# Performance work log

Measured on AMD Instinct MI355X. Metric: run time of the kernel, lower is better.

Reference implementation:

```python
import jax, jax.numpy as jnp
import numpy as np
from jax import lax


def setup_inputs() -> dict:
    key = jax.random.key(0)
    ks = jax.random.split(key, 9)
    B, Hh, Ww, Cin, Cout, F, E = 8, 64, 64, 256, 256, 128, 256
    s = 0.02  # glorot-ish scale to keep the H->pow(-0.5) chain numerically sane
    return {
        "x": jax.random.normal(ks[0], (B, Hh, Ww, Cin), jnp.float32),
        "w_phi": jax.random.normal(ks[1], (Cin, F), jnp.float32) * s,
        "b_phi": jnp.zeros((F,), jnp.float32),
        "w_a": jax.random.normal(ks[2], (Cin, F), jnp.float32) * s,
        "b_a": jnp.zeros((F,), jnp.float32),
        "w_m": jax.random.normal(ks[3], (7, 7, Cin, E), jnp.float32) * s,
        "b_m": jnp.zeros((E,), jnp.float32),
        "weight_2": jax.random.normal(ks[4], (Cin, Cout), jnp.float32) * s,
        "bias_2": jnp.zeros((Cout,), jnp.float32),
    }


def reference(x, w_phi, b_phi, w_a, b_a, w_m, b_m, weight_2, bias_2):
    B, Hh, Ww, Cin = x.shape
    V = Hh * Ww
    F = w_phi.shape[1]
    E = w_m.shape[-1]

    # phi: 1x1 conv -> [B, V, F]
    phi = (jnp.einsum('bhwc,cf->bhwf', x, w_phi) + b_phi).reshape(B, V, F)

    # A: global average pool + 1x1 conv -> diagonal scale vector [B, F]
    a = jnp.mean(x, axis=(1, 2)) @ w_a + b_a  # (B, F)

    # M: 7x7 SAME conv -> [B, V, E]
    M = lax.conv_general_dilated(
        x, w_m, window_strides=(1, 1), padding='SAME',
        dimension_numbers=('NHWC', 'HWIO', 'NHWC')) + b_m
    M = M.reshape(B, V, E)

    # H = |phi @ diag(a) @ phi^T @ M| without materializing diag(a)
    t = jnp.einsum('bvf,bve->bfe', phi, M)        # phi^T @ M : (B, F, E)
    t = a[:, :, None] * t                          # diag(a) scaling
    Hmat = jnp.abs(jnp.einsum('bvf,bfe->bve', phi, t))  # (B, V, E)

    D = jnp.sum(Hmat, axis=2)                      # vertex degree (B, V)
    D_H = D[:, :, None] ** -0.5 * Hmat             # D^{-1/2} H
    Binv = 1.0 / jnp.sum(Hmat, axis=1)             # edge degree inverse (B, E)

    feats = x.reshape(B, V, Cin)
    tmp = jnp.einsum('bve,bvc->bec', D_H, feats)   # D_H^T @ features
    tmp = Binv[:, :, None] * tmp                   # diag(B^{-1}) scaling
    agg = jnp.einsum('bve,bec->bvc', D_H, tmp)     # D_H @ ...

    out = (feats - agg) @ weight_2 + bias_2        # (B, V, Cout)
    return out.reshape(B, Hh, Ww, -1)
```

## Files before the change

### kernel.cpp

```cpp
#include <hip/hip_runtime.h>
#include <hip/hip_bf16.h>

typedef unsigned short u16;
typedef unsigned int u32;
#define DI __device__ __forceinline__

typedef __attribute__((ext_vector_type(8))) short v8s;
typedef __attribute__((ext_vector_type(4))) float v4f;

constexpr int B_ = 8;
constexpr int V_ = 4096;
constexpr int C_ = 256;
constexpr int F_ = 128;
constexpr int E_ = 256;
constexpr int KK_ = 49;
constexpr int PWS = 80;
constexpr int PS  = 5600;

constexpr size_t OFF_XSUM   = 0;
constexpr size_t OFF_CSUM   = 2048;
constexpr size_t OFF_SPHI   = 4096;
constexpr size_t OFF_A      = 5120;
constexpr size_t OFF_T      = 6144;
constexpr size_t OFF_TMPT   = 268288;
constexpr size_t ZERO_HEAD  = 792576;
constexpr size_t OFF_TT16   = 792576;
constexpr size_t OFF_T2T16  = 923648;
constexpr size_t OFF_W2T16  = 1185792;
constexpr size_t OFF_PHIT   = 1218560;
constexpr size_t OFF_XPT    = 3315712;
constexpr size_t XPT_FLOATS = 5734400;
constexpr size_t OFF_WMT    = 9050112;

DI float bf2f(u16 u) {
    union { u32 i; float f; } v; v.i = ((u32)u) << 16; return v.f;
}
DI u16 f2bf(float f) {
    union { float f; u32 i; } v; v.f = f;
    u32 r = v.i + 0x7fff + ((v.i >> 16) & 1);
    return (u16)(r >> 16);
}

__global__ void k_xsum(const float* __restrict__ x, float* __restrict__ ws) {
    int b = blockIdx.x >> 3;
    int chunk = blockIdx.x & 7;
    int c = threadIdx.x;
    const float* xb = x + ((size_t)b * V_ + chunk * 512) * C_ + c;
    float s = 0.f;
    for (int v = 0; v < 512; ++v) s += xb[(size_t)v * C_];
    atomicAdd(&ws[OFF_XSUM + b * C_ + c], s);
}

__global__ void k_a(const float* __restrict__ w_a, const float* __restrict__ b_a,
                    float* __restrict__ ws) {
    int b = blockIdx.x, f = threadIdx.x;
    float acc = b_a[f];
    const float* xs = &ws[OFF_XSUM + b * C_];
    for (int c = 0; c < C_; ++c)
        acc += (xs[c] * (1.0f / 4096.0f)) * w_a[c * F_ + f];
    ws[OFF_A + b * F_ + f] = acc;
}

__global__ void k_phi(const float* __restrict__ x, const float* __restrict__ w_phi,
                      const float* __restrict__ b_phi, float* __restrict__ ws) {
    __shared__ float xsT[C_][8];
    int r0 = blockIdx.x * 8;
    int b = r0 >> 12;
    int v0 = r0 & 4095;
    int tid = threadIdx.x;
    const float* xb = x + (size_t)r0 * C_;
    for (int i = tid; i < 8 * C_; i += 128) xsT[i & 255][i >> 8] = xb[i];
    __syncthreads();
    int f = tid;
    float bp = b_phi[f];
    float acc[8];
#pragma unroll
    for (int r = 0; r < 8; ++r) acc[r] = bp;
    const float* wp = w_phi + f;
    for (int c = 0; c < C_; ++c) {
        float w = wp[c * F_];
        float4 xa = *(const float4*)&xsT[c][0];
        float4 xb4 = *(const float4*)&xsT[c][4];
        acc[0] += xa.x * w;  acc[1] += xa.y * w;  acc[2] += xa.z * w;  acc[3] += xa.w * w;
        acc[4] += xb4.x * w; acc[5] += xb4.y * w; acc[6] += xb4.z * w; acc[7] += xb4.w * w;
    }
    u16 pb[8];
    float ssum = 0.f;
#pragma unroll
    for (int r = 0; r < 8; ++r) { pb[r] = f2bf(acc[r]); ssum += acc[r]; }
    u16* phiT = (u16*)&ws[OFF_PHIT];
    uint4 q;
    q.x = (u32)pb[0] | ((u32)pb[1] << 16);
    q.y = (u32)pb[2] | ((u32)pb[3] << 16);
    q.z = (u32)pb[4] | ((u32)pb[5] << 16);
    q.w = (u32)pb[6] | ((u32)pb[7] << 16);
    *(uint4*)(phiT + ((size_t)(b * F_ + f)) * V_ + v0) = q;
    atomicAdd(&ws[OFF_SPHI + b * F_ + f], ssum);
}

__global__ void k_padx(const float* __restrict__ x, float* __restrict__ ws) {
    __shared__ float tile[64][68];
    int b = blockIdx.x >> 6;
    int h = blockIdx.x & 63;
    int tid = threadIdx.x;
    u16* xpt = (u16*)&ws[OFF_XPT];
    for (int cc = 0; cc < 4; ++cc) {
        int c0 = cc * 64;
        int w = tid >> 2, q = tid & 3;
        const float* xr = x + ((size_t)(b * V_ + h * 64 + w)) * C_ + c0 + q * 16;
        float4 f0 = *(const float4*)(xr);
        float4 f1 = *(const float4*)(xr + 4);
        float4 f2 = *(const float4*)(xr + 8);
        float4 f3 = *(const float4*)(xr + 12);
        __syncthreads();
        *(float4*)&tile[w][q * 16]      = f0;
        *(float4*)&tile[w][q * 16 + 4]  = f1;
        *(float4*)&tile[w][q * 16 + 8]  = f2;
        *(float4*)&tile[w][q * 16 + 12] = f3;
        __syncthreads();
        int c = tid >> 2, j4 = tid & 3;
        u16* dst = xpt + ((size_t)(b * C_ + c0 + c)) * PS + (h + 3) * PWS + 3 + j4 * 16;
#pragma unroll
        for (int ww = 0; ww < 16; ++ww) dst[ww] = f2bf(tile[j4 * 16 + ww][c]);
    }
}

__global__ void k_wmt(const float* __restrict__ w_m, float* __restrict__ ws) {
    int kk = blockIdx.x;
    int e = threadIdx.x;
    u16* wmt = (u16*)&ws[OFF_WMT];
    for (int c0 = 0; c0 < C_; c0 += 8) {
        u16 pk[8];
#pragma unroll
        for (int i = 0; i < 8; ++i)
            pk[i] = f2bf(w_m[((size_t)kk * C_ + c0 + i) * E_ + e]);
        uint4 q;
        q.x = (u32)pk[0] | ((u32)pk[1] << 16);
        q.y = (u32)pk[2] | ((u32)pk[3] << 16);
        q.z = (u32)pk[4] | ((u32)pk[5] << 16);
        q.w = (u32)pk[6] | ((u32)pk[7] << 16);
        *(uint4*)(wmt + ((size_t)(kk * E_ + e)) * C_ + c0) = q;
    }
}

__global__ void k_w2t(const float* __restrict__ w2, float* __restrict__ ws) {
    int co = blockIdx.x, c = threadIdx.x;
    ((u16*)&ws[OFF_W2T16])[(size_t)co * C_ + c] = f2bf(w2[(size_t)c * C_ + co]);
}

template <int KX>
DI void g1_loop(const u16* __restrict__ phiT_b, const u16* __restrict__ xpt_b,
                int ky, u16* lds_a, u16* lds_b, int tid, v4f acc[4][4]) {
    int wave = tid >> 6, lane = tid & 63, quad = lane >> 4, l15 = lane & 15;
    int mi2 = wave >> 2, ni2 = wave & 3;
    int fA = tid >> 2, vsA = (tid & 3) * 8;
    int cB = tid >> 1, sB = (tid & 1) * 16;
    const u16* bbase = xpt_b + (size_t)cB * PS + (size_t)ky * PWS + sB;
    constexpr int J0 = KX >> 1;
#pragma unroll 1
    for (int chunk = 0; chunk < 128; ++chunk) {
        int v0 = chunk * 32;
        int h = chunk >> 1, w0 = (chunk & 1) * 32;
        uint4 a4 = *(const uint4*)(phiT_b + (size_t)fA * V_ + v0 + vsA);
        const u16* bp = bbase + h * PWS + w0;
        uint4 q0 = *(const uint4*)(bp);
        uint4 q1 = *(const uint4*)(bp + 8);
        u32 dw[12];
        dw[0] = q0.x; dw[1] = q0.y; dw[2] = q0.z; dw[3] = q0.w;
        dw[4] = q1.x; dw[5] = q1.y; dw[6] = q1.z; dw[7] = q1.w;
        if constexpr (KX >= 1) {
            uint4 q2 = *(const uint4*)(bp + 16);
            dw[8] = q2.x; dw[9] = q2.y; dw[10] = q2.z; dw[11] = q2.w;
        } else {
            dw[8] = dw[9] = dw[10] = dw[11] = 0;
        }
        u32 o[8];
        if constexpr ((KX & 1) == 0) {
#pragma unroll
            for (int i = 0; i < 8; ++i) o[i] = dw[J0 + i];
        } else {
#pragma unroll
            for (int i = 0; i < 8; ++i) o[i] = (dw[J0 + i] >> 16) | (dw[J0 + i + 1] << 16);
        }
        u16* la = lds_a + (chunk & 1) * (128 * 40);
        u16* lb = lds_b + (chunk & 1) * (256 * 40);
        *(uint4*)&la[fA * 40 + vsA] = a4;
        *(uint4*)&lb[cB * 40 + sB]     = (uint4){o[0], o[1], o[2], o[3]};
        *(uint4*)&lb[cB * 40 + sB + 8] = (uint4){o[4], o[5], o[6], o[7]};
        __syncthreads();
        v8s afr[4], bfr[4];
#pragma unroll
        for (int ai = 0; ai < 4; ++ai)
            afr[ai] = *(const v8s*)&la[(mi2 * 64 + ai * 16 + l15) * 40 + quad * 8];
#pragma unroll
        for (int bi = 0; bi < 4; ++bi)
            bfr[bi] = *(const v8s*)&lb[(ni2 * 64 + bi * 16 + l15) * 40 + quad * 8];
#pragma unroll
        for (int ai = 0; ai < 4; ++ai)
#pragma unroll
            for (int bi = 0; bi < 4; ++bi)
                acc[ai][bi] = __builtin_amdgcn_mfma_f32_16x16x32_bf16(
                    afr[ai], bfr[bi], acc[ai][bi], 0, 0, 0);
    }
}

__global__ __launch_bounds__(512, 2) void k_gemm1(const float* __restrict__ ws_c,
                                                  u16* __restrict__ G) {
    __shared__ u16 lds_a[2 * 128 * 40];
    __shared__ u16 lds_b[2 * 256 * 40];
    int b  = blockIdx.x & 7;
    int kk = blockIdx.x >> 3;
    int ky = kk / 7, kx = kk % 7;
    int tid = threadIdx.x;
    int wave = tid >> 6, lane = tid & 63, quad = lane >> 4, l15 = lane & 15;
    int mi2 = wave >> 2, ni2 = wave & 3;
    const u16* phiT_b = (const u16*)&ws_c[OFF_PHIT] + (size_t)b * F_ * V_;
    const u16* xpt_b  = (const u16*)&ws_c[OFF_XPT] + (size_t)b * C_ * PS;
    v4f acc[4][4];
#pragma unroll
    for (int i = 0; i < 4; ++i)
#pragma unroll
        for (int j = 0; j < 4; ++j) acc[i][j] = (v4f){0.f, 0.f, 0.f, 0.f};
    switch (kx) {
        case 0: g1_loop<0>(phiT_b, xpt_b, ky, lds_a, lds_b, tid, acc); break;
        case 1: g1_loop<1>(phiT_b, xpt_b, ky, lds_a, lds_b, tid, acc); break;
        case 2: g1_loop<2>(phiT_b, xpt_b, ky, lds_a, lds_b, tid, acc); break;
        case 3: g1_loop<3>(phiT_b, xpt_b, ky, lds_a, lds_b, tid, acc); break;
        case 4: g1_loop<4>(phiT_b, xpt_b, ky, lds_a, lds_b, tid, acc); break;
        case 5: g1_loop<5>(phiT_b, xpt_b, ky, lds_a, lds_b, tid, acc); break;
        case 6: g1_loop<6>(phiT_b, xpt_b, ky, lds_a, lds_b, tid, acc); break;
    }
    u16* Gb = G + ((size_t)(b * KK_ + kk)) * F_ * C_;
#pragma unroll
    for (int ai = 0; ai < 4; ++ai)
#pragma unroll
        for (int bi = 0; bi < 4; ++bi) {
            int c = ni2 * 64 + bi * 16 + l15;
#pragma unroll
            for (int r = 0; r < 4; ++r) {
                int f = mi2 * 64 + ai * 16 + quad * 4 + r;
                Gb[(size_t)f * C_ + c] = f2bf(acc[ai][bi][r]);
            }
        }
}

__global__ void k_gemm2(const u16* __restrict__ G, float* __restrict__ ws) {
    int blk = blockIdx.x;
    int kg = blk % 7; blk /= 7;
    int ei = blk % 4; blk /= 4;
    int fi = blk % 2; int b = blk / 2;
    int tid = threadIdx.x;
    int wave = tid >> 6, lane = tid & 63, quad = lane >> 4, l15 = lane & 15;
    int fbase = fi * 64 + wave * 16;
    int ebase = ei * 64;
    const u16* wmt = (const u16*)&ws[OFF_WMT];
    const u16* Gb = G + (size_t)b * KK_ * F_ * C_;
    v4f acc[4];
#pragma unroll
    for (int i = 0; i < 4; ++i) acc[i] = (v4f){0.f, 0.f, 0.f, 0.f};
    for (int kk = kg * 7; kk < kg * 7 + 7; ++kk) {
        const u16* Ga = Gb + ((size_t)kk * F_ + fbase + l15) * C_;
        const u16* Wb = wmt + ((size_t)kk * E_ + ebase + l15) * C_;
#pragma unroll 2
        for (int cs = 0; cs < 8; ++cs) {
            v8s af = *(const v8s*)(Ga + cs * 32 + quad * 8);
#pragma unroll
            for (int nt = 0; nt < 4; ++nt) {
                v8s bf = *(const v8s*)(Wb + (size_t)nt * 16 * C_ + cs * 32 + quad * 8);
                acc[nt] = __builtin_amdgcn_mfma_f32_16x16x32_bf16(af, bf, acc[nt], 0, 0, 0);
            }
        }
    }
#pragma unroll
    for (int nt = 0; nt < 4; ++nt)
#pragma unroll
        for (int r = 0; r < 4; ++r) {
            int e = ebase + nt * 16 + l15;
            int f = fbase + quad * 4 + r;
            atomicAdd(&ws[OFF_T + ((size_t)(b * E_ + e)) * F_ + f], acc[nt][r]);
        }
}

__global__ void k_tfix(const float* __restrict__ b_m, float* __restrict__ ws) {
    int b = blockIdx.x >> 8, e = blockIdx.x & 255, f = threadIdx.x;
    float av = ws[OFF_A + b * F_ + f];
    float sp = ws[OFF_SPHI + b * F_ + f];
    float t = av * (ws[OFF_T + ((size_t)(b * E_ + e)) * F_ + f] + sp * b_m[e]);
    ((u16*)&ws[OFF_TT16])[((size_t)(b * E_ + e)) * F_ + f] = f2bf(t);
}

__global__ void k_hd(float* __restrict__ ws) {
    __shared__ u16 phiL[64 * 136];
    __shared__ float cspart[4][E_];
    int b = blockIdx.x >> 6;
    int chunkIdx = blockIdx.x & 63;
    int v0 = chunkIdx * 64;
    int tid = threadIdx.x;
    {
        int f = tid & 127, seg = (tid >> 7) * 32;
        const u16* src = (const u16*)&ws[OFF_PHIT] + ((size_t)(b * F_ + f)) * V_ + v0 + seg;
        uint4 q0 = *(const uint4*)(src);
        uint4 q1 = *(const uint4*)(src + 8);
        uint4 q2 = *(const uint4*)(src + 16);
        uint4 q3 = *(const uint4*)(src + 24);
        u32 dw[16] = {q0.x, q0.y, q0.z, q0.w, q1.x, q1.y, q1.z, q1.w,
                      q2.x, q2.y, q2.z, q2.w, q3.x, q3.y, q3.z, q3.w};
#pragma unroll
        for (int j = 0; j < 16; ++j) {
            phiL[(seg + 2 * j) * 136 + f]     = (u16)(dw[j] & 0xffff);
            phiL[(seg + 2 * j + 1) * 136 + f] = (u16)(dw[j] >> 16);
        }
    }
    __syncthreads();
    int wave = tid >> 6, lane = tid & 63, quad = lane >> 4, l15 = lane & 15;
    const u16* tt = (const u16*)&ws[OFF_TT16] + (size_t)b * E_ * F_;
    v4f acc[16];
#pragma unroll
    for (int i = 0; i < 16; ++i) acc[i] = (v4f){0.f, 0.f, 0.f, 0.f};
#pragma unroll
    for (int kc = 0; kc < 4; ++kc) {
        v8s af = *(const v8s*)&phiL[(wave * 16 + l15) * 136 + kc * 32 + quad * 8];
#pragma unroll
        for (int nt = 0; nt < 16; ++nt) {
            v8s bf = *(const v8s*)(tt + (size_t)(nt * 16 + l15) * F_ + kc * 32 + quad * 8);
            acc[nt] = __builtin_amdgcn_mfma_f32_16x16x32_bf16(af, bf, acc[nt], 0, 0, 0);
        }
    }
#pragma unroll
    for (int nt = 0; nt < 16; ++nt)
#pragma unroll
        for (int r = 0; r < 4; ++r) acc[nt][r] = fabsf(acc[nt][r]);
    v4f rs = acc[0];
#pragma unroll
    for (int nt = 1; nt < 16; ++nt) rs += acc[nt];
#pragma unroll
    for (int m = 1; m < 16; m <<= 1) {
#pragma unroll
        for (int r = 0; r < 4; ++r) rs[r] += __shfl_xor(rs[r], m, 64);
    }
    float rsd[4];
#pragma unroll
    for (int r = 0; r < 4; ++r) rsd[r] = rsqrtf(rs[r]);
#pragma unroll
    for (int nt = 0; nt < 16; ++nt) {
        float cs = acc[nt][0] + acc[nt][1] + acc[nt][2] + acc[nt][3];
        cs += __shfl_xor(cs, 16, 64);
        cs += __shfl_xor(cs, 32, 64);
        if (quad == 0) cspart[wave][nt * 16 + l15] = cs;
    }
    u16* hm = (u16*)&ws[OFF_XPT];
#pragma unroll
    for (int nt = 0; nt < 16; ++nt)
#pragma unroll
        for (int r = 0; r < 4; ++r) {
            int v = v0 + wave * 16 + quad * 4 + r;
            hm[((size_t)(b * V_ + v)) * E_ + nt * 16 + l15] = f2bf(acc[nt][r] * rsd[r]);
        }
    __syncthreads();
    {
        int e = tid;
        float s = cspart[0][e] + cspart[1][e] + cspart[2][e] + cspart[3][e];
        ws[OFF_T + ((size_t)(b * 64 + chunkIdx)) * E_ + e] = s;
    }
}

__global__ void k_csum(float* __restrict__ ws) {
    int b = blockIdx.x, e = threadIdx.x;
    const float* p = &ws[OFF_T + (size_t)b * 64 * E_ + e];
    float s = 0.f;
    for (int i = 0; i < 64; ++i) s += p[(size_t)i * E_];
    ws[OFF_CSUM + b * E_ + e] = s;
}

__global__ __launch_bounds__(512, 2) void k_tmp(const float* __restrict__ x,
                                                float* __restrict__ ws) {
    __shared__ u16 xT[256 * 40];
    __shared__ u16 hT[128 * 40];
    int blk = blockIdx.x;
    int eh = blk & 1; blk >>= 1;
    int vs = blk & 15; int b = blk >> 4;
    int v0b = vs * 256;
    int tid = threadIdx.x;
    int wave = tid >> 6, lane = tid & 63, quad = lane >> 4, l15 = lane & 15;
    int m0 = wave * 32;
    const u16* hmS = (const u16*)&ws[OFF_XPT];
    v4f acc[2][8];
#pragma unroll
    for (int i = 0; i < 2; ++i)
#pragma unroll
        for (int j = 0; j < 8; ++j) acc[i][j] = (v4f){0.f, 0.f, 0.f, 0.f};
    int sv = tid & 31, sg = tid >> 5;
#pragma unroll 1
    for (int ch = 0; ch < 8; ++ch) {
        int vbase = v0b + ch * 32;
        const float* xr = x + ((size_t)(b * V_ + vbase + sv)) * C_ + sg * 16;
        float4 xf0 = *(const float4*)(xr);
        float4 xf1 = *(const float4*)(xr + 4);
        float4 xf2 = *(const float4*)(xr + 8);
        float4 xf3 = *(const float4*)(xr + 12);
        const u16* hr = hmS + ((size_t)(b * V_ + vbase + sv)) * E_ + eh * 128 + sg * 8;
        uint4 hq = *(const uint4*)hr;
        u16 hp[8] = {(u16)(hq.x & 0xffff), (u16)(hq.x >> 16), (u16)(hq.y & 0xffff),
                     (u16)(hq.y >> 16), (u16)(hq.z & 0xffff), (u16)(hq.z >> 16),
                     (u16)(hq.w & 0xffff), (u16)(hq.w >> 16)};
        float xv[16] = {xf0.x, xf0.y, xf0.z, xf0.w, xf1.x, xf1.y, xf1.z, xf1.w,
                        xf2.x, xf2.y, xf2.z, xf2.w, xf3.x, xf3.y, xf3.z, xf3.w};
        __syncthreads();
#pragma unroll
        for (int i = 0; i < 16; ++i) xT[(sg * 16 + i) * 40 + sv] = f2bf(xv[i]);
#pragma unroll
        for (int i = 0; i < 8; ++i) hT[(sg * 8 + i) * 40 + sv] = hp[i];
        __syncthreads();
        v8s a0 = *(const v8s*)&xT[(m0 + l15) * 40 + quad * 8];
        v8s a1 = *(const v8s*)&xT[(m0 + 16 + l15) * 40 + quad * 8];
#pragma unroll
        for (int nt = 0; nt < 8; ++nt) {
            v8s bf = *(const v8s*)&hT[(nt * 16 + l15) * 40 + quad * 8];
            acc[0][nt] = __builtin_amdgcn_mfma_f32_16x16x32_bf16(a0, bf, acc[0][nt], 0, 0, 0);
            acc[1][nt] = __builtin_amdgcn_mfma_f32_16x16x32_bf16(a1, bf, acc[1][nt], 0, 0, 0);
        }
    }
#pragma unroll
    for (int mt = 0; mt < 2; ++mt)
#pragma unroll
        for (int nt = 0; nt < 8; ++nt)
#pragma unroll
            for (int r = 0; r < 4; ++r) {
                int c = m0 + mt * 16 + quad * 4 + r;
                int e = eh * 128 + nt * 16 + l15;
                atomicAdd(&ws[OFF_TMPT + ((size_t)(b * C_ + c)) * E_ + e], acc[mt][nt][r]);
            }
}

__global__ void k_t2fix(float* __restrict__ ws) {
    int b = blockIdx.x >> 8, c = blockIdx.x & 255, e = threadIdx.x;
    float binv = 1.0f / ws[OFF_CSUM + b * E_ + e];
    float tv = ws[OFF_TMPT + ((size_t)(b * C_ + c)) * E_ + e];
    ((u16*)&ws[OFF_T2T16])[((size_t)(b * C_ + c)) * E_ + e] = f2bf(tv * binv);
}

__global__ __launch_bounds__(256, 2) void k_out(const float* __restrict__ x,
                                                const float* __restrict__ b2,
                                                const float* __restrict__ ws,
                                                float* __restrict__ io) {
    __shared__ u16 dL[64 * 264];
    int b = blockIdx.x >> 6;
    int v0 = (blockIdx.x & 63) * 64;
    int tid = threadIdx.x;
    int wave = tid >> 6, lane = tid & 63, quad = lane >> 4, l15 = lane & 15;
    const u16* hm = (const u16*)&ws[OFF_XPT] + ((size_t)(b * V_ + v0 + wave * 16 + l15)) * E_;
    const u16* t2 = (const u16*)&ws[OFF_T2T16] + (size_t)b * C_ * E_;
    v4f acc[16];
#pragma unroll
    for (int i = 0; i < 16; ++i) acc[i] = (v4f){0.f, 0.f, 0.f, 0.f};
#pragma unroll 2
    for (int kc = 0; kc < 8; ++kc) {
        v8s af = *(const v8s*)(hm + kc * 32 + quad * 8);
#pragma unroll
        for (int nt = 0; nt < 16; ++nt) {
            v8s bf = *(const v8s*)(t2 + (size_t)(nt * 16 + l15) * E_ + kc * 32 + quad * 8);
            acc[nt] = __builtin_amdgcn_mfma_f32_16x16x32_bf16(af, bf, acc[nt], 0, 0, 0);
        }
    }
#pragma unroll
    for (int nt = 0; nt < 16; ++nt)
#pragma unroll
        for (int r = 0; r < 4; ++r) {
            int v = wave * 16 + quad * 4 + r;
            int c = nt * 16 + l15;
            float xv = x[((size_t)(b * V_ + v0 + v)) * C_ + c];
            dL[v * 264 + c] = f2bf(xv - acc[nt][r]);
        }
    __syncthreads();
    const u16* w2t = (const u16*)&ws[OFF_W2T16];
    v4f acc2[16];
#pragma unroll
    for (int i = 0; i < 16; ++i) acc2[i] = (v4f){0.f, 0.f, 0.f, 0.f};
#pragma unroll 2
    for (int kc = 0; kc < 8; ++kc) {
        v8s af = *(const v8s*)&dL[(wave * 16 + l15) * 264 + kc * 32 + quad * 8];
#pragma unroll
        for (int nt = 0; nt < 16; ++nt) {
            v8s bf = *(const v8s*)(w2t + (size_t)(nt * 16 + l15) * C_ + kc * 32 + quad * 8);
            acc2[nt] = __builtin_amdgcn_mfma_f32_16x16x32_bf16(af, bf, acc2[nt], 0, 0, 0);
        }
    }
#pragma unroll
    for (int nt = 0; nt < 16; ++nt)
#pragma unroll
        for (int r = 0; r < 4; ++r) {
            int v = wave * 16 + quad * 4 + r;
            int co = nt * 16 + l15;
            io[((size_t)(b * V_ + v0 + v)) * C_ + co] = acc2[nt][r] + b2[co];
        }
}

extern "C" void kernel_launch(void* const* d_in, const int* in_sizes, int n_in,
                              void* d_out, int out_size, void* d_ws, size_t ws_size,
                              hipStream_t stream) {
    const float* x     = (const float*)d_in[0];
    const float* w_phi = (const float*)d_in[1];
    const float* b_phi = (const float*)d_in[2];
    const float* w_a   = (const float*)d_in[3];
    const float* b_a   = (const float*)d_in[4];
    const float* w_m   = (const float*)d_in[5];
    const float* b_m   = (const float*)d_in[6];
    const float* w2    = (const float*)d_in[7];
    const float* b2    = (const float*)d_in[8];
    float* ws = (float*)d_ws;
    float* io = (float*)d_out;

    hipMemsetAsync(ws, 0, ZERO_HEAD * sizeof(float), stream);
    hipMemsetAsync(ws + OFF_XPT, 0, XPT_FLOATS * sizeof(float), stream);
    k_xsum<<<dim3(64), dim3(256), 0, stream>>>(x, ws);
    k_a<<<dim3(8), dim3(128), 0, stream>>>(w_a, b_a, ws);
    k_phi<<<dim3(4096), dim3(128), 0, stream>>>(x, w_phi, b_phi, ws);
    k_padx<<<dim3(512), dim3(256), 0, stream>>>(x, ws);
    k_wmt<<<dim3(49), dim3(256), 0, stream>>>(w_m, ws);
    k_w2t<<<dim3(256), dim3(256), 0, stream>>>(w2, ws);
    k_gemm1<<<dim3(392), dim3(512), 0, stream>>>(ws, (u16*)d_out);
    k_gemm2<<<dim3(448), dim3(256), 0, stream>>>((const u16*)d_out, ws);
    k_tfix<<<dim3(2048), dim3(128), 0, stream>>>(b_m, ws);
    k_hd<<<dim3(512), dim3(256), 0, stream>>>(ws);
    k_csum<<<dim3(8), dim3(256), 0, stream>>>(ws);
    k_tmp<<<dim3(256), dim3(512), 0, stream>>>(x, ws);
    k_t2fix<<<dim3(2048), dim3(256), 0, stream>>>(ws);
    k_out<<<dim3(512), dim3(256), 0, stream>>>(x, b2, ws, io);
}
```

Baseline: 603.5 us.

## Software-pipeline gemm1 global loads with MFMA and widen xsum grid

The gemm1 inner loop now prefetches the next chunk's phiT and padded-x tiles into registers before running the MFMAs on the current LDS buffer, then writes the prefetched data into the other LDS buffer, with one barrier per iteration. The aim is to hide global-load latency behind matrix math instead of stalling on loads before each barrier. Separately, k_xsum is split into 256 blocks of 128 rows instead of 64 blocks of 512 rows, giving more parallelism for the channel-sum reduction at the cost of more atomics. The prefetch raises register pressure under launch_bounds(512,2) and issues one redundant load on the last iteration.

```diff
diff --git a/kernel.cpp b/kernel.cpp
--- a/kernel.cpp
+++ b/kernel.cpp
@@ -42,12 +42,12 @@
 }
 
 __global__ void k_xsum(const float* __restrict__ x, float* __restrict__ ws) {
-    int b = blockIdx.x >> 3;
-    int chunk = blockIdx.x & 7;
+    int b = blockIdx.x >> 5;
+    int chunk = blockIdx.x & 31;
     int c = threadIdx.x;
-    const float* xb = x + ((size_t)b * V_ + chunk * 512) * C_ + c;
+    const float* xb = x + ((size_t)b * V_ + chunk * 128) * C_ + c;
     float s = 0.f;
-    for (int v = 0; v < 512; ++v) s += xb[(size_t)v * C_];
+    for (int v = 0; v < 128; ++v) s += xb[(size_t)v * C_];
     atomicAdd(&ws[OFF_XSUM + b * C_ + c], s);
 }
 
@@ -149,45 +149,61 @@
 }
 
 template <int KX>
+DI void g1_load(const u16* __restrict__ pAr, const u16* __restrict__ bbase, int chunk,
+                uint4& a4, u32 dw[12]) {
+    int v0 = chunk * 32;
+    a4 = *(const uint4*)(pAr + v0);
+    const u16* bp = bbase + (chunk >> 1) * PWS + (chunk & 1) * 32;
+    uint4 q0 = *(const uint4*)(bp);
+    uint4 q1 = *(const uint4*)(bp + 8);
+    dw[0] = q0.x; dw[1] = q0.y; dw[2] = q0.z; dw[3] = q0.w;
+    dw[4] = q1.x; dw[5] = q1.y; dw[6] = q1.z; dw[7] = q1.w;
+    if constexpr (KX >= 1) {
+        uint4 q2 = *(const uint4*)(bp + 16);
+        dw[8] = q2.x; dw[9] = q2.y; dw[10] = q2.z; dw[11] = q2.w;
+    } else {
+        dw[8] = dw[9] = dw[10] = dw[11] = 0;
+    }
+}
+
+template <int KX>
+DI void g1_shift(const u32 dw[12], u32 o[8]) {
+    constexpr int J0 = KX >> 1;
+    if constexpr ((KX & 1) == 0) {
+#pragma unroll
+        for (int i = 0; i < 8; ++i) o[i] = dw[J0 + i];
+    } else {
+#pragma unroll
+        for (int i = 0; i < 8; ++i) o[i] = (dw[J0 + i] >> 16) | (dw[J0 + i + 1] << 16);
+    }
+}
+
+template <int KX>
 DI void g1_loop(const u16* __restrict__ phiT_b, const u16* __restrict__ xpt_b,
                 int ky, u16* lds_a, u16* lds_b, int tid, v4f acc[4][4]) {
     int wave = tid >> 6, lane = tid & 63, quad = lane >> 4, l15 = lane & 15;
     int mi2 = wave >> 2, ni2 = wave & 3;
     int fA = tid >> 2, vsA = (tid & 3) * 8;
     int cB = tid >> 1, sB = (tid & 1) * 16;
+    const u16* pAr = phiT_b + (size_t)fA * V_ + vsA;
     const u16* bbase = xpt_b + (size_t)cB * PS + (size_t)ky * PWS + sB;
-    constexpr int J0 = KX >> 1;
+    {
+        uint4 a4; u32 dw[12];
+        g1_load<KX>(pAr, bbase, 0, a4, dw);
+        u32 o[8];
+        g1_shift<KX>(dw, o);
+        *(uint4*)&lds_a[fA * 40 + vsA] = a4;
+        *(uint4*)&lds_b[cB * 40 + sB]     = (uint4){o[0], o[1], o[2], o[3]};
+        *(uint4*)&lds_b[cB * 40 + sB + 8] = (uint4){o[4], o[5], o[6], o[7]};
+    }
+    __syncthreads();
 #pragma unroll 1
     for (int chunk = 0; chunk < 128; ++chunk) {
-        int v0 = chunk * 32;
-        int h = chunk >> 1, w0 = (chunk & 1) * 32;
-        uint4 a4 = *(const uint4*)(phiT_b + (size_t)fA * V_ + v0 + vsA);
-        const u16* bp = bbase + h * PWS + w0;
-        uint4 q0 = *(const uint4*)(bp);
-        uint4 q1 = *(const uint4*)(bp + 8);
-        u32 dw[12];
-        dw[0] = q0.x; dw[1] = q0.y; dw[2] = q0.z; dw[3] = q0.w;
-        dw[4] = q1.x; dw[5] = q1.y; dw[6] = q1.z; dw[7] = q1.w;
-        if constexpr (KX >= 1) {
-            uint4 q2 = *(const uint4*)(bp + 16);
-            dw[8] = q2.x; dw[9] = q2.y; dw[10] = q2.z; dw[11] = q2.w;
-        } else {
-            dw[8] = dw[9] = dw[10] = dw[11] = 0;
-        }
-        u32 o[8];
-        if constexpr ((KX & 1) == 0) {
-#pragma unroll
-            for (int i = 0; i < 8; ++i) o[i] = dw[J0 + i];
-        } else {
-#pragma unroll
-            for (int i = 0; i < 8; ++i) o[i] = (dw[J0 + i] >> 16) | (dw[J0 + i + 1] << 16);
-        }
-        u16* la = lds_a + (chunk & 1) * (128 * 40);
-        u16* lb = lds_b + (chunk & 1) * (256 * 40);
-        *(uint4*)&la[fA * 40 + vsA] = a4;
-        *(uint4*)&lb[cB * 40 + sB]     = (uint4){o[0], o[1], o[2], o[3]};
-        *(uint4*)&lb[cB * 40 + sB + 8] = (uint4){o[4], o[5], o[6], o[7]};
-        __syncthreads();
+        int cn = (chunk + 1 < 128) ? chunk + 1 : 127;
+        uint4 a4; u32 dw[12];
+        g1_load<KX>(pAr, bbase, cn, a4, dw);
+        const u16* la = lds_a + (chunk & 1) * (128 * 40);
+        const u16* lb = lds_b + (chunk & 1) * (256 * 40);
         v8s afr[4], bfr[4];
 #pragma unroll
         for (int ai = 0; ai < 4; ++ai)
@@ -201,6 +217,14 @@
             for (int bi = 0; bi < 4; ++bi)
                 acc[ai][bi] = __builtin_amdgcn_mfma_f32_16x16x32_bf16(
                     afr[ai], bfr[bi], acc[ai][bi], 0, 0, 0);
+        u32 o[8];
+        g1_shift<KX>(dw, o);
+        u16* lan = lds_a + ((chunk + 1) & 1) * (128 * 40);
+        u16* lbn = lds_b + ((chunk + 1) & 1) * (256 * 40);
+        *(uint4*)&lan[fA * 40 + vsA] = a4;
+        *(uint4*)&lbn[cB * 40 + sB]     = (uint4){o[0], o[1], o[2], o[3]};
+        *(uint4*)&lbn[cB * 40 + sB + 8] = (uint4){o[4], o[5], o[6], o[7]};
+        __syncthreads();
     }
 }
 
@@ -512,7 +536,7 @@
 
     hipMemsetAsync(ws, 0, ZERO_HEAD * sizeof(float), stream);
     hipMemsetAsync(ws + OFF_XPT, 0, XPT_FLOATS * sizeof(float), stream);
-    k_xsum<<<dim3(64), dim3(256), 0, stream>>>(x, ws);
+    k_xsum<<<dim3(256), dim3(256), 0, stream>>>(x, ws);
     k_a<<<dim3(8), dim3(128), 0, stream>>>(w_a, b_a, ws);
     k_phi<<<dim3(4096), dim3(128), 0, stream>>>(x, w_phi, b_phi, ws);
     k_padx<<<dim3(512), dim3(256), 0, stream>>>(x, ws);
```

Result: no change. 592.8 us (-1.8%).
